# Optimization experiments

Measured on AMD Instinct MI355X. Metric: run time of the kernel, lower is better.

The kernel has to match this reference:

```python
import jax, jax.numpy as jnp
import numpy as np

H = 128   # local_channels (hidden_size)
I = 128   # global_channels (input_size)
T = 30    # future_steps
M = 6     # num_modes
N = 8192  # num agents
MIN_SCALE = 0.001
LN_EPS = 1e-5


def layernorm(x, g, b):
    mu = jnp.mean(x, axis=-1, keepdims=True)
    var = jnp.var(x, axis=-1, keepdims=True)
    return (x - mu) * jax.lax.rsqrt(var + LN_EPS) * g + b


def setup_inputs() -> dict:
    key = jax.random.key(0)
    ks = jax.random.split(key, 24)

    def rn(k, shape, s=0.02):
        return jax.random.normal(k, shape, dtype=jnp.float32) * s

    return {
        "local_embed": jax.random.normal(ks[0], (N, H), jnp.float32),
        "global_embed": jax.random.normal(ks[1], (M, N, I), jnp.float32),
        # GRU params (PyTorch layout: gates ordered r, z, n)
        "W_ih": rn(ks[2], (3 * H, I)), "W_hh": rn(ks[3], (3 * H, H)),
        "b_ih": jnp.zeros((3 * H,), jnp.float32), "b_hh": jnp.zeros((3 * H,), jnp.float32),
        # loc head: Linear(H,H) -> LN -> ReLU -> Linear(H,2)
        "loc1_w": rn(ks[4], (H, H)), "loc1_b": jnp.zeros((H,), jnp.float32),
        "loc_ln_g": jnp.ones((H,), jnp.float32), "loc_ln_b": jnp.zeros((H,), jnp.float32),
        "loc2_w": rn(ks[5], (2, H)), "loc2_b": jnp.zeros((2,), jnp.float32),
        # scale head: same structure
        "sc1_w": rn(ks[6], (H, H)), "sc1_b": jnp.zeros((H,), jnp.float32),
        "sc_ln_g": jnp.ones((H,), jnp.float32), "sc_ln_b": jnp.zeros((H,), jnp.float32),
        "sc2_w": rn(ks[7], (2, H)), "sc2_b": jnp.zeros((2,), jnp.float32),
        # pi head: Linear(H+I,H)->LN->ReLU->Linear(H,H)->LN->ReLU->Linear(H,1)
        "pi1_w": rn(ks[8], (H, H + I)), "pi1_b": jnp.zeros((H,), jnp.float32),
        "pi_ln1_g": jnp.ones((H,), jnp.float32), "pi_ln1_b": jnp.zeros((H,), jnp.float32),
        "pi2_w": rn(ks[9], (H, H)), "pi2_b": jnp.zeros((H,), jnp.float32),
        "pi_ln2_g": jnp.ones((H,), jnp.float32), "pi_ln2_b": jnp.zeros((H,), jnp.float32),
        "pi3_w": rn(ks[10], (1, H)), "pi3_b": jnp.zeros((1,), jnp.float32),
    }


def reference(local_embed, global_embed, W_ih, W_hh, b_ih, b_hh,
              loc1_w, loc1_b, loc_ln_g, loc_ln_b, loc2_w, loc2_b,
              sc1_w, sc1_b, sc_ln_g, sc_ln_b, sc2_w, sc2_b,
              pi1_w, pi1_b, pi_ln1_g, pi_ln1_b, pi2_w, pi2_b,
              pi_ln2_g, pi_ln2_b, pi3_w, pi3_b):
    # pi head: cat(broadcast local [M,N,H], global [M,N,I]) -> MLP -> [N, M]
    pi_in = jnp.concatenate(
        (jnp.broadcast_to(local_embed, (M, N, H)), global_embed), axis=-1)
    h1 = jax.nn.relu(layernorm(pi_in @ pi1_w.T + pi1_b, pi_ln1_g, pi_ln1_b))
    h2 = jax.nn.relu(layernorm(h1 @ pi2_w.T + pi2_b, pi_ln2_g, pi_ln2_b))
    pi = (h2 @ pi3_w.T + pi3_b)[..., 0].T  # [N, M]

    # GRU: input is the SAME x at every timestep -> precompute input gates once
    x = global_embed.reshape(M * N, I)                  # [B, I], B = M*N
    gx = x @ W_ih.T + b_ih                              # [B, 3H]
    xr, xz, xn = jnp.split(gx, 3, axis=-1)
    h0 = jnp.tile(local_embed, (M, 1))                  # [B, H]

    def step(h, _):
        gh = h @ W_hh.T + b_hh
        hr, hz, hn = jnp.split(gh, 3, axis=-1)
        r = jax.nn.sigmoid(xr + hr)
        z = jax.nn.sigmoid(xz + hz)
        n = jnp.tanh(xn + r * hn)
        h_new = (1.0 - z) * n + z * h
        return h_new, h_new

    _, outs = jax.lax.scan(step, h0, None, length=T)    # [T, B, H]
    out = jnp.transpose(outs, (1, 0, 2))                # [B, T, H]

    loc = jax.nn.relu(layernorm(out @ loc1_w.T + loc1_b, loc_ln_g, loc_ln_b)) @ loc2_w.T + loc2_b
    sc = jax.nn.relu(layernorm(out @ sc1_w.T + sc1_b, sc_ln_g, sc_ln_b)) @ sc2_w.T + sc2_b
    scale = jax.nn.elu(sc) + 1.0 + MIN_SCALE

    traj = jnp.concatenate((loc, scale), axis=-1).reshape(M, N, T, 4)
    return traj, pi
```

## Files before the change

kernel.cpp:

```cpp
#include <hip/hip_runtime.h>
#include <math.h>

#define H 128
#define I_DIM 128
#define T_STEPS 30
#define M_MODES 6
#define N_AG 8192
#define B_TOT (M_MODES * N_AG)
#define LN_EPS 1e-5f
#define MIN_SCALE 0.001f
#define LOG2E 1.44269504088896f

typedef short bf16x8 __attribute__((ext_vector_type(8)));
typedef float f32x4 __attribute__((ext_vector_type(4)));

#define MFMA16x16x32(A, B, C) __builtin_amdgcn_mfma_f32_16x16x32_bf16(A, B, C, 0, 0, 0)

__device__ __forceinline__ short f2b(float f) {
    union { float f; unsigned u; } v; v.f = f;
    return (short)((v.u + 0x7FFFu + ((v.u >> 16) & 1u)) >> 16);
}

__device__ __forceinline__ bf16x8 load8_cvt(const float* __restrict__ p) {
    const float4 a = ((const float4*)p)[0];
    const float4 b = ((const float4*)p)[1];
    bf16x8 r;
    r[0]=f2b(a.x); r[1]=f2b(a.y); r[2]=f2b(a.z); r[3]=f2b(a.w);
    r[4]=f2b(b.x); r[5]=f2b(b.y); r[6]=f2b(b.z); r[7]=f2b(b.w);
    return r;
}

__device__ __forceinline__ bf16x8 load8_cvt_s(const float* __restrict__ p, float s) {
    const float4 a = ((const float4*)p)[0];
    const float4 b = ((const float4*)p)[1];
    bf16x8 r;
    r[0]=f2b(a.x*s); r[1]=f2b(a.y*s); r[2]=f2b(a.z*s); r[3]=f2b(a.w*s);
    r[4]=f2b(b.x*s); r[5]=f2b(b.y*s); r[6]=f2b(b.z*s); r[7]=f2b(b.w*s);
    return r;
}

__device__ __forceinline__ float sigm2(float xp) {
    return __builtin_amdgcn_rcpf(1.f + __builtin_amdgcn_exp2f(-xp));
}
__device__ __forceinline__ float tanh2(float yp) {
    return 1.f - 2.f * __builtin_amdgcn_rcpf(1.f + __builtin_amdgcn_exp2f(yp));
}

#define DPP_ADD(v, ctrl)                                                     \
    v += __builtin_bit_cast(float, __builtin_amdgcn_mov_dpp(                 \
             __builtin_bit_cast(int, v), ctrl, 0xF, 0xF, true))

__device__ __forceinline__ float red16(float v) {
    DPP_ADD(v, 0xB1);
    DPP_ADD(v, 0x4E);
    DPP_ADD(v, 0x124);
    DPP_ADD(v, 0x128);
    return v;
}

__global__ __launch_bounds__(256, 2) void gx_kernel(
    const float* __restrict__ global_embed,
    const float* __restrict__ W_ih, const float* __restrict__ b_ih,
    const float* __restrict__ b_hh,
    int base, int ntiles, int Rc, float* __restrict__ gx_ws)
{
    __shared__ short xbuf[16][136];

    const int tid = threadIdx.x;
    const int w  = tid >> 6;
    const int l  = tid & 63;
    const int ln = l & 15;
    const int lg = l >> 4;

    bf16x8 wf[6][4];
    float bias[6];
    #pragma unroll
    for (int nt = 0; nt < 6; ++nt) {
        const int ch = 96*w + 16*nt + ln;
        const float sc = (ch < 2*H) ? LOG2E : (2.f * LOG2E);
        #pragma unroll
        for (int kt = 0; kt < 4; ++kt)
            wf[nt][kt] = load8_cvt_s(W_ih + (size_t)ch * I_DIM + kt*32 + lg*8, sc);
        bias[nt] = (b_ih[ch] + (ch < 2*H ? b_hh[ch] : 0.f)) * sc;
    }

    const int s_r = tid >> 4, s_sg = tid & 15;

    for (int it = blockIdx.x; it < ntiles; it += gridDim.x) {
        const int r0 = it * 16;
        __syncthreads();
        {
            const float* src = global_embed + (size_t)(base + r0 + s_r) * I_DIM + s_sg*8;
            const float4 a = ((const float4*)src)[0];
            const float4 c = ((const float4*)src)[1];
            short tmp[8];
            tmp[0]=f2b(a.x); tmp[1]=f2b(a.y); tmp[2]=f2b(a.z); tmp[3]=f2b(a.w);
            tmp[4]=f2b(c.x); tmp[5]=f2b(c.y); tmp[6]=f2b(c.z); tmp[7]=f2b(c.w);
            *(uint4*)&xbuf[s_r][s_sg*8] = *(uint4*)tmp;
        }
        __syncthreads();

        bf16x8 af[4];
        #pragma unroll
        for (int kt = 0; kt < 4; ++kt)
            af[kt] = *(const bf16x8*)&xbuf[ln][kt*32 + lg*8];

        f32x4 acc[6];
        #pragma unroll
        for (int nt = 0; nt < 6; ++nt) acc[nt] = (f32x4)(0.f);
        #pragma unroll
        for (int kt = 0; kt < 4; ++kt)
            #pragma unroll
            for (int nt = 0; nt < 6; ++nt)
                acc[nt] = MFMA16x16x32(af[kt], wf[nt][kt], acc[nt]);

        #pragma unroll
        for (int nt = 0; nt < 6; ++nt) {
            const f32x4 v = acc[nt] + (f32x4)(bias[nt]);
            *(f32x4*)(gx_ws + (size_t)(96*w + 16*nt + ln) * Rc + r0 + lg*4) = v;
        }
    }
}

#define PI_INBF_OFF   0
#define PI_H1_OFF     33792
#define PI_REDL_OFF   51200
#define PI_RED3_OFF   53248
#define SM_BYTES      54272

__global__ __launch_bounds__(512, 2) void fused_kernel(
    const float* __restrict__ local_embed, const float* __restrict__ gx_ws,
    const float* __restrict__ W_hh, const float* __restrict__ b_hh,
    int base, int ntiles, int Rc, int F,
    const float* __restrict__ loc1_w, const float* __restrict__ loc1_b,
    const float* __restrict__ loc_ln_g, const float* __restrict__ loc_ln_b,
    const float* __restrict__ loc2_w, const float* __restrict__ loc2_b,
    const float* __restrict__ sc1_w, const float* __restrict__ sc1_b,
    const float* __restrict__ sc_ln_g, const float* __restrict__ sc_ln_b,
    const float* __restrict__ sc2_w, const float* __restrict__ sc2_b,
    float* __restrict__ traj,
    const float* __restrict__ global_embed,
    const float* __restrict__ pi1_w, const float* __restrict__ pi1_b,
    const float* __restrict__ ln1_g, const float* __restrict__ ln1_b,
    const float* __restrict__ pi2_w, const float* __restrict__ pi2_b,
    const float* __restrict__ ln2_g, const float* __restrict__ ln2_b,
    const float* __restrict__ pi3_w, const float* __restrict__ pi3_b,
    float* __restrict__ pi_out)
{
    __shared__ __align__(16) char smraw[SM_BYTES];

    const int tid = threadIdx.x;
    const int w  = tid >> 6;
    const int l  = tid & 63;
    const int ln = l & 15;
    const int lg = l >> 4;

    if ((int)blockIdx.x < F) {
        short (*hb0p)[136] = (short(*)[136])smraw;
        short (*hb1p)[136] = (short(*)[136])(smraw + 8704);

        if (w < 4) {
            bf16x8 wf[3][2][4];
            float bhn[2];
            #pragma unroll
            for (int u = 0; u < 2; ++u) {
                const int c = 32*w + 16*u + ln;
                bhn[u] = b_hh[2*H + c] * (2.f * LOG2E);
                #pragma unroll
                for (int g = 0; g < 3; ++g) {
                    const int crow = g*H + c;
                    const float sc = (g < 2) ? LOG2E : (2.f * LOG2E);
                    #pragma unroll
                    for (int kt = 0; kt < 4; ++kt)
                        wf[g][u][kt] = load8_cvt_s(W_hh + (size_t)crow * H + kt*32 + lg*8, sc);
                }
            }

            for (int it = blockIdx.x; it < ntiles; it += F) {
                const int lb0 = it * 32;
                __syncthreads();

                {
                    const int r  = tid >> 3;
                    const int sg = tid & 7;
                    const int b = base + lb0 + r;
                    const int n = b & (N_AG - 1);
                    const float* src = local_embed + (size_t)n * H;
                    #pragma unroll
                    for (int hseg = 0; hseg < 2; ++hseg) {
                        const int s8 = sg + hseg*8;
                        const float4 a = ((const float4*)(src + s8*8))[0];
                        const float4 c = ((const float4*)(src + s8*8))[1];
                        short tmp[8];
                        tmp[0]=f2b(a.x); tmp[1]=f2b(a.y); tmp[2]=f2b(a.z); tmp[3]=f2b(a.w);
                        tmp[4]=f2b(c.x); tmp[5]=f2b(c.y); tmp[6]=f2b(c.z); tmp[7]=f2b(c.w);
                        *(uint4*)&hb0p[r][s8*8] = *(uint4*)tmp;
                    }
                }

                float h_reg[2][2][4];
                #pragma unroll
                for (int grp = 0; grp < 2; ++grp)
                    #pragma unroll
                    for (int u = 0; u < 2; ++u) {
                        const int j = 32*w + 16*u + ln;
                        #pragma unroll
                        for (int rg = 0; rg < 4; ++rg) {
                            const int b = base + lb0 + grp*16 + lg*4 + rg;
                            const int n = b & (N_AG - 1);
                            h_reg[grp][u][rg] = local_embed[(size_t)n * H + j];
                        }
                    }
                float gx[2][3][2][4];
                #pragma unroll
                for (int grp = 0; grp < 2; ++grp)
                    #pragma unroll
                    for (int g = 0; g < 3; ++g)
                        #pragma unroll
                        for (int u = 0; u < 2; ++u) {
                            const int ch = g*128 + 32*w + 16*u + ln;
                            const f32x4 v = *(const f32x4*)(gx_ws + (size_t)ch * Rc + lb0 + grp*16 + lg*4);
                            #pragma unroll
                            for (int rg = 0; rg < 4; ++rg) gx[grp][g][u][rg] = v[rg];
                        }
                __syncthreads();

                int cur = 0;
                for (int i = 0; i <= T_STEPS; ++i) {
                    if (i < T_STEPS) {
                        short (*hc)[136] = cur ? hb1p : hb0p;
                        short (*hx)[136] = cur ? hb0p : hb1p;
                        #pragma unroll
                        for (int grp = 0; grp < 2; ++grp) {
                            bf16x8 af[4];
                            #pragma unroll
                            for (int kt = 0; kt < 4; ++kt)
                                af[kt] = *(const bf16x8*)&hc[grp*16 + ln][kt*32 + lg*8];

                            f32x4 ga[3][2];
                            #pragma unroll
                            for (int g = 0; g < 3; ++g)
                                #pragma unroll
                                for (int u = 0; u < 2; ++u) ga[g][u] = (f32x4)(0.f);
                            #pragma unroll
                            for (int kt = 0; kt < 4; ++kt)
                                #pragma unroll
                                for (int g = 0; g < 3; ++g)
                                    #pragma unroll
                                    for (int u = 0; u < 2; ++u)
                                        ga[g][u] = MFMA16x16x32(af[kt], wf[g][u][kt], ga[g][u]);

                            #pragma unroll
                            for (int u = 0; u < 2; ++u) {
                                const int j = 32*w + 16*u + ln;
                                #pragma unroll
                                for (int rg = 0; rg < 4; ++rg) {
                                    const float rr = sigm2(gx[grp][0][u][rg] + ga[0][u][rg]);
                                    const float zz = sigm2(gx[grp][1][u][rg] + ga[1][u][rg]);
                                    const float nn = tanh2(gx[grp][2][u][rg] + rr * (ga[2][u][rg] + bhn[u]));
                                    const float h  = nn + zz * (h_reg[grp][u][rg] - nn);
                                    h_reg[grp][u][rg] = h;
                                    hx[grp*16 + lg*4 + rg][j] = f2b(h);
                                }
                            }
                        }
                    }
                    __syncthreads();
                    cur ^= 1;
                }
            }
        } else {
            const int hw = w - 4;
            const int hd = hw & 1;
            const int mrow = (hw >> 1) * 16;

            const float* __restrict__ W1  = hd ? sc1_w   : loc1_w;
            const float* __restrict__ B1v = hd ? sc1_b   : loc1_b;
            const float* __restrict__ Gv  = hd ? sc_ln_g : loc_ln_g;
            const float* __restrict__ Bv  = hd ? sc_ln_b : loc_ln_b;
            const float* __restrict__ W2  = hd ? sc2_w   : loc2_w;
            const float* __restrict__ B2v = hd ? sc2_b   : loc2_b;

            bf16x8 whf[8][4];
            float bias1[8], lng[8], lnb[8], w2a[8], w2b[8];
            #pragma unroll
            for (int nt = 0; nt < 8; ++nt) {
                const int c = 16*nt + ln;
                #pragma unroll
                for (int kt = 0; kt < 4; ++kt)
                    whf[nt][kt] = load8_cvt(W1 + (size_t)c * H + kt*32 + lg*8);
                bias1[nt] = B1v[c]; lng[nt] = Gv[c]; lnb[nt] = Bv[c];
                w2a[nt] = W2[c];    w2b[nt] = W2[H + c];
            }
            const float b2_0 = B2v[0], b2_1 = B2v[1];

            for (int it = blockIdx.x; it < ntiles; it += F) {
                const int lb0 = it * 32;
                __syncthreads();
                __syncthreads();

                int cur = 0;
                for (int i = 0; i <= T_STEPS; ++i) {
                    if (i >= 1) {
                        short (*hc)[136] = cur ? hb1p : hb0p;
                        bf16x8 af[4];
                        #pragma unroll
                        for (int kt = 0; kt < 4; ++kt)
                            af[kt] = *(const bf16x8*)&hc[mrow + ln][kt*32 + lg*8];

                        f32x4 acc[8];
                        #pragma unroll
                        for (int nt = 0; nt < 8; ++nt) acc[nt] = (f32x4)(0.f);
                        #pragma unroll
                        for (int kt = 0; kt < 4; ++kt)
                            #pragma unroll
                            for (int nt = 0; nt < 8; ++nt)
                                acc[nt] = MFMA16x16x32(af[kt], whf[nt][kt], acc[nt]);

                        const int t = i - 1;
                        #pragma unroll
                        for (int rg = 0; rg < 4; ++rg) {
                            float s = 0.f, q = 0.f;
                            #pragma unroll
                            for (int nt = 0; nt < 8; ++nt) {
                                const float a = acc[nt][rg] + bias1[nt];
                                acc[nt][rg] = a;
                                s += a; q += a*a;
                            }
                            s = red16(s);
                            q = red16(q);
                            const float mu = s * (1.f/H);
                            const float var = q * (1.f/H) - mu*mu;
                            const float rs = rsqrtf(var + LN_EPS);
                            const float murs = mu * rs;
                            float p0 = 0.f, p1 = 0.f;
                            #pragma unroll
                            for (int nt = 0; nt < 8; ++nt) {
                                float v = fmaf(fmaf(acc[nt][rg], rs, -murs), lng[nt], lnb[nt]);
                                v = fmaxf(v, 0.f);
                                p0 = fmaf(v, w2a[nt], p0);
                                p1 = fmaf(v, w2b[nt], p1);
                            }
                            p0 = red16(p0);
                            p1 = red16(p1);
                            if (ln == 0) {
                                const int b = base + lb0 + mrow + lg*4 + rg;
                                float v0 = p0 + b2_0;
                                float v1 = p1 + b2_1;
                                if (hd) {
                                    v0 = (v0 > 0.f ? v0 : expm1f(v0)) + 1.0f + MIN_SCALE;
                                    v1 = (v1 > 0.f ? v1 : expm1f(v1)) + 1.0f + MIN_SCALE;
                                }
                                *(float2*)(traj + ((size_t)b * T_STEPS + t) * 4 + hd*2) = make_float2(v0, v1);
                            }
                        }
                    }
                    __syncthreads();
                    cur ^= 1;
                }
            }
        }
        return;
    }

    {
        const int pbid = blockIdx.x - F;
        const int pgrid = gridDim.x - F;
        const int sub  = tid >> 8;
        const int stid = tid & 255;
        const int w4 = stid >> 6;

        short (*inbf)[264] = (short(*)[264])(smraw + PI_INBF_OFF + (size_t)sub*16896);
        short (*h1bf)[136] = (short(*)[136])(smraw + PI_H1_OFF   + (size_t)sub*8704);
        float (*redL)[32][2] = (float(*)[32][2])(smraw + PI_REDL_OFF + (size_t)sub*1024);
        float (*red3)[32]    = (float(*)[32])(smraw + PI_RED3_OFF + (size_t)sub*512);

        bf16x8 wf1[2][8];
        bf16x8 wf2[2][4];
        float b1[2], g1[2], bb1[2], b2[2], g2[2], bb2[2], w3[2];
        #pragma unroll
        for (int nt = 0; nt < 2; ++nt) {
            const int c = 32*w4 + 16*nt + ln;
            #pragma unroll
            for (int kt = 0; kt < 8; ++kt)
                wf1[nt][kt] = load8_cvt(pi1_w + (size_t)c * (2*H) + kt*32 + lg*8);
            #pragma unroll
            for (int kt = 0; kt < 4; ++kt)
                wf2[nt][kt] = load8_cvt(pi2_w + (size_t)c * H + kt*32 + lg*8);
            b1[nt] = pi1_b[c]; g1[nt] = ln1_g[c]; bb1[nt] = ln1_b[c];
            b2[nt] = pi2_b[c]; g2[nt] = ln2_g[c]; bb2[nt] = ln2_b[c];
            w3[nt] = pi3_w[c];
        }
        const float b3 = pi3_b[0];

        const int npairs = (B_TOT / 32) / 2;

        for (int p = pbid; p < npairs; p += pgrid) {
            const int r0 = (p*2 + sub) * 32;
            {
                const int r   = stid >> 3;
                const int seg = stid & 7;
                const int b = r0 + r;
                const int n = b & (N_AG - 1);
                const float* src = (seg < 4) ? (local_embed + (size_t)n * H + seg * 32)
                                             : (global_embed + (size_t)b * I_DIM + (seg - 4) * 32);
                short tmp[32];
                #pragma unroll
                for (int i = 0; i < 8; ++i) {
                    const float4 v = ((const float4*)src)[i];
                    tmp[i*4+0]=f2b(v.x); tmp[i*4+1]=f2b(v.y); tmp[i*4+2]=f2b(v.z); tmp[i*4+3]=f2b(v.w);
                }
                #pragma unroll
                for (int i = 0; i < 4; ++i)
                    *(uint4*)&inbf[r][seg*32 + i*8] = *(uint4*)&tmp[i*8];
            }
            __syncthreads();

            f32x4 acc1[2][2];
            #pragma unroll
            for (int m = 0; m < 2; ++m) {
                #pragma unroll
                for (int nt = 0; nt < 2; ++nt) acc1[m][nt] = (f32x4)(0.f);
                bf16x8 af[8];
                #pragma unroll
                for (int kt = 0; kt < 8; ++kt)
                    af[kt] = *(const bf16x8*)&inbf[m*16 + ln][kt*32 + lg*8];
                #pragma unroll
                for (int kt = 0; kt < 8; ++kt)
                    #pragma unroll
                    for (int nt = 0; nt < 2; ++nt)
                        acc1[m][nt] = MFMA16x16x32(af[kt], wf1[nt][kt], acc1[m][nt]);
            }

            #pragma unroll
            for (int m = 0; m < 2; ++m)
                #pragma unroll
                for (int rg = 0; rg < 4; ++rg) {
                    float s = 0.f, q = 0.f;
                    #pragma unroll
                    for (int nt = 0; nt < 2; ++nt) {
                        const float a = acc1[m][nt][rg] + b1[nt];
                        acc1[m][nt][rg] = a;
                        s += a; q += a*a;
                    }
                    s = red16(s);
                    q = red16(q);
                    if (ln == 0) {
                        const int row = m*16 + lg*4 + rg;
                        redL[w4][row][0] = s;
                        redL[w4][row][1] = q;
                    }
                }
            __syncthreads();

            #pragma unroll
            for (int m = 0; m < 2; ++m)
                #pragma unroll
                for (int rg = 0; rg < 4; ++rg) {
                    const int row = m*16 + lg*4 + rg;
                    const float S = redL[0][row][0] + redL[1][row][0] + redL[2][row][0] + redL[3][row][0];
                    const float Q = redL[0][row][1] + redL[1][row][1] + redL[2][row][1] + redL[3][row][1];
                    const float mu = S * (1.f/H);
                    const float var = Q * (1.f/H) - mu*mu;
                    const float rs = rsqrtf(var + LN_EPS);
                    #pragma unroll
                    for (int nt = 0; nt < 2; ++nt) {
                        const float v = fmaxf((acc1[m][nt][rg] - mu) * rs * g1[nt] + bb1[nt], 0.f);
                        h1bf[row][32*w4 + 16*nt + ln] = f2b(v);
                    }
                }
            __syncthreads();

            f32x4 acc2[2][2];
            #pragma unroll
            for (int m = 0; m < 2; ++m) {
                #pragma unroll
                for (int nt = 0; nt < 2; ++nt) acc2[m][nt] = (f32x4)(0.f);
                bf16x8 af[4];
                #pragma unroll
                for (int kt = 0; kt < 4; ++kt)
                    af[kt] = *(const bf16x8*)&h1bf[m*16 + ln][kt*32 + lg*8];
                #pragma unroll
                for (int kt = 0; kt < 4; ++kt)
                    #pragma unroll
                    for (int nt = 0; nt < 2; ++nt)
                        acc2[m][nt] = MFMA16x16x32(af[kt], wf2[nt][kt], acc2[m][nt]);
            }

            #pragma unroll
            for (int m = 0; m < 2; ++m)
                #pragma unroll
                for (int rg = 0; rg < 4; ++rg) {
                    float s = 0.f, q = 0.f;
                    #pragma unroll
                    for (int nt = 0; nt < 2; ++nt) {
                        const float a = acc2[m][nt][rg] + b2[nt];
                        acc2[m][nt][rg] = a;
                        s += a; q += a*a;
                    }
                    s = red16(s);
                    q = red16(q);
                    if (ln == 0) {
                        const int row = m*16 + lg*4 + rg;
                        redL[w4][row][0] = s;
                        redL[w4][row][1] = q;
                    }
                }
            __syncthreads();

            #pragma unroll
            for (int m = 0; m < 2; ++m)
                #pragma unroll
                for (int rg = 0; rg < 4; ++rg) {
                    const int row = m*16 + lg*4 + rg;
                    const float S = redL[0][row][0] + redL[1][row][0] + redL[2][row][0] + redL[3][row][0];
                    const float Q = redL[0][row][1] + redL[1][row][1] + redL[2][row][1] + redL[3][row][1];
                    const float mu = S * (1.f/H);
                    const float var = Q * (1.f/H) - mu*mu;
                    const float rs = rsqrtf(var + LN_EPS);
                    float p2 = 0.f;
                    #pragma unroll
                    for (int nt = 0; nt < 2; ++nt) {
                        const float v = fmaxf((acc2[m][nt][rg] - mu) * rs * g2[nt] + bb2[nt], 0.f);
                        p2 = fmaf(v, w3[nt], p2);
                    }
                    p2 = red16(p2);
                    if (ln == 0) red3[w4][row] = p2;
                }
            __syncthreads();

            if (stid < 32) {
                const int row = stid;
                const float pv = red3[0][row] + red3[1][row] + red3[2][row] + red3[3][row] + b3;
                const int b = r0 + row;
                const int n = b & (N_AG - 1);
                const int m = b >> 13;
                pi_out[(size_t)n * M_MODES + m] = pv;
            }
            __syncthreads();
        }
    }
}

extern "C" void kernel_launch(void* const* d_in, const int* in_sizes, int n_in,
                              void* d_out, int out_size, void* d_ws, size_t ws_size,
                              hipStream_t stream) {
    (void)in_sizes; (void)n_in; (void)out_size;
    const float* local_embed  = (const float*)d_in[0];
    const float* global_embed = (const float*)d_in[1];
    const float* W_ih   = (const float*)d_in[2];
    const float* W_hh   = (const float*)d_in[3];
    const float* b_ih   = (const float*)d_in[4];
    const float* b_hh   = (const float*)d_in[5];
    const float* loc1_w = (const float*)d_in[6];
    const float* loc1_b = (const float*)d_in[7];
    const float* loc_ln_g = (const float*)d_in[8];
    const float* loc_ln_b = (const float*)d_in[9];
    const float* loc2_w = (const float*)d_in[10];
    const float* loc2_b = (const float*)d_in[11];
    const float* sc1_w  = (const float*)d_in[12];
    const float* sc1_b  = (const float*)d_in[13];
    const float* sc_ln_g = (const float*)d_in[14];
    const float* sc_ln_b = (const float*)d_in[15];
    const float* sc2_w  = (const float*)d_in[16];
    const float* sc2_b  = (const float*)d_in[17];
    const float* pi1_w  = (const float*)d_in[18];
    const float* pi1_b  = (const float*)d_in[19];
    const float* pi_ln1_g = (const float*)d_in[20];
    const float* pi_ln1_b = (const float*)d_in[21];
    const float* pi2_w  = (const float*)d_in[22];
    const float* pi2_b  = (const float*)d_in[23];
    const float* pi_ln2_g = (const float*)d_in[24];
    const float* pi_ln2_b = (const float*)d_in[25];
    const float* pi3_w  = (const float*)d_in[26];
    const float* pi3_b  = (const float*)d_in[27];

    float* traj = (float*)d_out;
    float* pi_out = traj + (size_t)B_TOT * T_STEPS * 4;

    const size_t row_bytes = 384 * sizeof(float);
    long long rc = (long long)(ws_size / row_bytes);
    int Rc = rc > B_TOT ? B_TOT : (int)rc;
    Rc &= ~31;

    if (Rc >= 32) {
        float* gx_ws = (float*)d_ws;
        bool first = true;

        for (int basep = 0; basep < B_TOT; basep += Rc) {
            const int rows = (B_TOT - basep < Rc) ? (B_TOT - basep) : Rc;

            const int gxtiles = rows / 16;
            gx_kernel<<<(gxtiles < 512 ? gxtiles : 512), 256, 0, stream>>>(
                global_embed, W_ih, b_ih, b_hh, basep, gxtiles, Rc, gx_ws);

            const int ntiles = rows / 32;
            int F = ntiles < 768 ? ntiles : 768;
            const int P = first ? 256 : 0;
            fused_kernel<<<F + P, 512, 0, stream>>>(
                local_embed, gx_ws, W_hh, b_hh, basep, ntiles, Rc, F,
                loc1_w, loc1_b, loc_ln_g, loc_ln_b, loc2_w, loc2_b,
                sc1_w, sc1_b, sc_ln_g, sc_ln_b, sc2_w, sc2_b, traj,
                global_embed,
                pi1_w, pi1_b, pi_ln1_g, pi_ln1_b,
                pi2_w, pi2_b, pi_ln2_g, pi_ln2_b, pi3_w, pi3_b, pi_out);
            first = false;
        }
    }
}
```

Baseline: 589.2 us.

## Fuse GRU input-gate GEMM into recurrent kernel and drop gx workspace

Removes the separate gx_kernel and its global workspace. Each recurrent tile now stages global_embed in LDS as bf16 (loaded by the head warps) and computes the input gates with MFMA, using W_ih fragments that are then overwritten by W_hh fragments in the same registers. Also switches bf16 conversion to packed v_cvt_pk_bf16_f32 and defers traj stores by one step so they overlap the next timestep. This trades a global round-trip of the 384-wide gx buffer and an extra launch for reloading and converting both weight matrices once per tile.

```diff
diff --git a/kernel.cpp b/kernel.cpp
--- a/kernel.cpp
+++ b/kernel.cpp
@@ -16,27 +16,34 @@
 
 #define MFMA16x16x32(A, B, C) __builtin_amdgcn_mfma_f32_16x16x32_bf16(A, B, C, 0, 0, 0)
 
+__device__ __forceinline__ unsigned cvt_pk(float lo, float hi) {
+    unsigned r;
+    asm("v_cvt_pk_bf16_f32 %0, %1, %2" : "=v"(r) : "v"(lo), "v"(hi));
+    return r;
+}
+
+__device__ __forceinline__ uint4 pack8(float4 a, float4 b) {
+    uint4 r;
+    r.x = cvt_pk(a.x, a.y); r.y = cvt_pk(a.z, a.w);
+    r.z = cvt_pk(b.x, b.y); r.w = cvt_pk(b.z, b.w);
+    return r;
+}
+
+__device__ __forceinline__ bf16x8 load8_cvt(const float* __restrict__ p) {
+    return __builtin_bit_cast(bf16x8, pack8(((const float4*)p)[0], ((const float4*)p)[1]));
+}
+
+__device__ __forceinline__ bf16x8 load8_cvt_s(const float* __restrict__ p, float s) {
+    float4 a = ((const float4*)p)[0];
+    float4 b = ((const float4*)p)[1];
+    a.x*=s; a.y*=s; a.z*=s; a.w*=s;
+    b.x*=s; b.y*=s; b.z*=s; b.w*=s;
+    return __builtin_bit_cast(bf16x8, pack8(a, b));
+}
+
 __device__ __forceinline__ short f2b(float f) {
     union { float f; unsigned u; } v; v.f = f;
     return (short)((v.u + 0x7FFFu + ((v.u >> 16) & 1u)) >> 16);
-}
-
-__device__ __forceinline__ bf16x8 load8_cvt(const float* __restrict__ p) {
-    const float4 a = ((const float4*)p)[0];
-    const float4 b = ((const float4*)p)[1];
-    bf16x8 r;
-    r[0]=f2b(a.x); r[1]=f2b(a.y); r[2]=f2b(a.z); r[3]=f2b(a.w);
-    r[4]=f2b(b.x); r[5]=f2b(b.y); r[6]=f2b(b.z); r[7]=f2b(b.w);
-    return r;
-}
-
-__device__ __forceinline__ bf16x8 load8_cvt_s(const float* __restrict__ p, float s) {
-    const float4 a = ((const float4*)p)[0];
-    const float4 b = ((const float4*)p)[1];
-    bf16x8 r;
-    r[0]=f2b(a.x*s); r[1]=f2b(a.y*s); r[2]=f2b(a.z*s); r[3]=f2b(a.w*s);
-    r[4]=f2b(b.x*s); r[5]=f2b(b.y*s); r[6]=f2b(b.z*s); r[7]=f2b(b.w*s);
-    return r;
 }
 
 __device__ __forceinline__ float sigm2(float xp) {
@@ -58,70 +65,8 @@
     return v;
 }
 
-__global__ __launch_bounds__(256, 2) void gx_kernel(
-    const float* __restrict__ global_embed,
-    const float* __restrict__ W_ih, const float* __restrict__ b_ih,
-    const float* __restrict__ b_hh,
-    int base, int ntiles, int Rc, float* __restrict__ gx_ws)
-{
-    __shared__ short xbuf[16][136];
-
-    const int tid = threadIdx.x;
-    const int w  = tid >> 6;
-    const int l  = tid & 63;
-    const int ln = l & 15;
-    const int lg = l >> 4;
-
-    bf16x8 wf[6][4];
-    float bias[6];
-    #pragma unroll
-    for (int nt = 0; nt < 6; ++nt) {
-        const int ch = 96*w + 16*nt + ln;
-        const float sc = (ch < 2*H) ? LOG2E : (2.f * LOG2E);
-        #pragma unroll
-        for (int kt = 0; kt < 4; ++kt)
-            wf[nt][kt] = load8_cvt_s(W_ih + (size_t)ch * I_DIM + kt*32 + lg*8, sc);
-        bias[nt] = (b_ih[ch] + (ch < 2*H ? b_hh[ch] : 0.f)) * sc;
-    }
-
-    const int s_r = tid >> 4, s_sg = tid & 15;
-
-    for (int it = blockIdx.x; it < ntiles; it += gridDim.x) {
-        const int r0 = it * 16;
-        __syncthreads();
-        {
-            const float* src = global_embed + (size_t)(base + r0 + s_r) * I_DIM + s_sg*8;
-            const float4 a = ((const float4*)src)[0];
-            const float4 c = ((const float4*)src)[1];
-            short tmp[8];
-            tmp[0]=f2b(a.x); tmp[1]=f2b(a.y); tmp[2]=f2b(a.z); tmp[3]=f2b(a.w);
-            tmp[4]=f2b(c.x); tmp[5]=f2b(c.y); tmp[6]=f2b(c.z); tmp[7]=f2b(c.w);
-            *(uint4*)&xbuf[s_r][s_sg*8] = *(uint4*)tmp;
-        }
-        __syncthreads();
-
-        bf16x8 af[4];
-        #pragma unroll
-        for (int kt = 0; kt < 4; ++kt)
-            af[kt] = *(const bf16x8*)&xbuf[ln][kt*32 + lg*8];
-
-        f32x4 acc[6];
-        #pragma unroll
-        for (int nt = 0; nt < 6; ++nt) acc[nt] = (f32x4)(0.f);
-        #pragma unroll
-        for (int kt = 0; kt < 4; ++kt)
-            #pragma unroll
-            for (int nt = 0; nt < 6; ++nt)
-                acc[nt] = MFMA16x16x32(af[kt], wf[nt][kt], acc[nt]);
-
-        #pragma unroll
-        for (int nt = 0; nt < 6; ++nt) {
-            const f32x4 v = acc[nt] + (f32x4)(bias[nt]);
-            *(f32x4*)(gx_ws + (size_t)(96*w + 16*nt + ln) * Rc + r0 + lg*4) = v;
-        }
-    }
-}
-
+#define HB0 0
+#define HB1 8704
 #define PI_INBF_OFF   0
 #define PI_H1_OFF     33792
 #define PI_REDL_OFF   51200
@@ -129,9 +74,10 @@
 #define SM_BYTES      54272
 
 __global__ __launch_bounds__(512, 2) void fused_kernel(
-    const float* __restrict__ local_embed, const float* __restrict__ gx_ws,
-    const float* __restrict__ W_hh, const float* __restrict__ b_hh,
-    int base, int ntiles, int Rc, int F,
+    const float* __restrict__ local_embed, const float* __restrict__ global_embed,
+    const float* __restrict__ W_ih, const float* __restrict__ W_hh,
+    const float* __restrict__ b_ih, const float* __restrict__ b_hh,
+    int ntiles, int F,
     const float* __restrict__ loc1_w, const float* __restrict__ loc1_b,
     const float* __restrict__ loc_ln_g, const float* __restrict__ loc_ln_b,
     const float* __restrict__ loc2_w, const float* __restrict__ loc2_b,
@@ -139,7 +85,6 @@
     const float* __restrict__ sc_ln_g, const float* __restrict__ sc_ln_b,
     const float* __restrict__ sc2_w, const float* __restrict__ sc2_b,
     float* __restrict__ traj,
-    const float* __restrict__ global_embed,
     const float* __restrict__ pi1_w, const float* __restrict__ pi1_b,
     const float* __restrict__ ln1_g, const float* __restrict__ ln1_b,
     const float* __restrict__ pi2_w, const float* __restrict__ pi2_b,
@@ -156,45 +101,38 @@
     const int lg = l >> 4;
 
     if ((int)blockIdx.x < F) {
-        short (*hb0p)[136] = (short(*)[136])smraw;
-        short (*hb1p)[136] = (short(*)[136])(smraw + 8704);
-
         if (w < 4) {
-            bf16x8 wf[3][2][4];
-            float bhn[2];
+            float bias_ih[3][2], bhn[2];
             #pragma unroll
             for (int u = 0; u < 2; ++u) {
                 const int c = 32*w + 16*u + ln;
                 bhn[u] = b_hh[2*H + c] * (2.f * LOG2E);
                 #pragma unroll
                 for (int g = 0; g < 3; ++g) {
-                    const int crow = g*H + c;
                     const float sc = (g < 2) ? LOG2E : (2.f * LOG2E);
-                    #pragma unroll
-                    for (int kt = 0; kt < 4; ++kt)
-                        wf[g][u][kt] = load8_cvt_s(W_hh + (size_t)crow * H + kt*32 + lg*8, sc);
-                }
-            }
+                    bias_ih[g][u] = (b_ih[g*H + c] + (g < 2 ? b_hh[g*H + c] : 0.f)) * sc;
+                }
+            }
+            const int ro = ln*272 + lg*16;
+            const int wb = (lg*4)*272 + (32*w + ln)*2;
+            const int sr_ = tid >> 3;
+            const int ssg = tid & 7;
+
+            bf16x8 wf[3][2][4];
 
             for (int it = blockIdx.x; it < ntiles; it += F) {
                 const int lb0 = it * 32;
                 __syncthreads();
 
                 {
-                    const int r  = tid >> 3;
-                    const int sg = tid & 7;
-                    const int b = base + lb0 + r;
-                    const int n = b & (N_AG - 1);
+                    const int n = (lb0 + sr_) & (N_AG - 1);
                     const float* src = local_embed + (size_t)n * H;
                     #pragma unroll
                     for (int hseg = 0; hseg < 2; ++hseg) {
-                        const int s8 = sg + hseg*8;
+                        const int s8 = ssg + hseg*8;
                         const float4 a = ((const float4*)(src + s8*8))[0];
                         const float4 c = ((const float4*)(src + s8*8))[1];
-                        short tmp[8];
-                        tmp[0]=f2b(a.x); tmp[1]=f2b(a.y); tmp[2]=f2b(a.z); tmp[3]=f2b(a.w);
-                        tmp[4]=f2b(c.x); tmp[5]=f2b(c.y); tmp[6]=f2b(c.z); tmp[7]=f2b(c.w);
-                        *(uint4*)&hb0p[r][s8*8] = *(uint4*)tmp;
+                        *(uint4*)(smraw + HB0 + sr_*272 + s8*16) = pack8(a, c);
                     }
                 }
 
@@ -206,36 +144,72 @@
                         const int j = 32*w + 16*u + ln;
                         #pragma unroll
                         for (int rg = 0; rg < 4; ++rg) {
-                            const int b = base + lb0 + grp*16 + lg*4 + rg;
-                            const int n = b & (N_AG - 1);
+                            const int n = (lb0 + grp*16 + lg*4 + rg) & (N_AG - 1);
                             h_reg[grp][u][rg] = local_embed[(size_t)n * H + j];
                         }
                     }
+
+                #pragma unroll
+                for (int u = 0; u < 2; ++u)
+                    #pragma unroll
+                    for (int g = 0; g < 3; ++g) {
+                        const int crow = g*H + 32*w + 16*u + ln;
+                        const float sc = (g < 2) ? LOG2E : (2.f * LOG2E);
+                        #pragma unroll
+                        for (int kt = 0; kt < 4; ++kt)
+                            wf[g][u][kt] = load8_cvt_s(W_ih + (size_t)crow * I_DIM + kt*32 + lg*8, sc);
+                    }
+                __syncthreads();
+
                 float gx[2][3][2][4];
                 #pragma unroll
-                for (int grp = 0; grp < 2; ++grp)
+                for (int grp = 0; grp < 2; ++grp) {
+                    bf16x8 ax[4];
+                    #pragma unroll
+                    for (int kt = 0; kt < 4; ++kt)
+                        ax[kt] = *(const bf16x8*)(smraw + HB1 + ro + grp*4352 + kt*64);
+                    f32x4 ag[3][2];
                     #pragma unroll
                     for (int g = 0; g < 3; ++g)
                         #pragma unroll
-                        for (int u = 0; u < 2; ++u) {
-                            const int ch = g*128 + 32*w + 16*u + ln;
-                            const f32x4 v = *(const f32x4*)(gx_ws + (size_t)ch * Rc + lb0 + grp*16 + lg*4);
-                            #pragma unroll
-                            for (int rg = 0; rg < 4; ++rg) gx[grp][g][u][rg] = v[rg];
-                        }
+                        for (int u = 0; u < 2; ++u) ag[g][u] = (f32x4)(0.f);
+                    #pragma unroll
+                    for (int kt = 0; kt < 4; ++kt)
+                        #pragma unroll
+                        for (int g = 0; g < 3; ++g)
+                            #pragma unroll
+                            for (int u = 0; u < 2; ++u)
+                                ag[g][u] = MFMA16x16x32(ax[kt], wf[g][u][kt], ag[g][u]);
+                    #pragma unroll
+                    for (int g = 0; g < 3; ++g)
+                        #pragma unroll
+                        for (int u = 0; u < 2; ++u)
+                            #pragma unroll
+                            for (int rg = 0; rg < 4; ++rg)
+                                gx[grp][g][u][rg] = ag[g][u][rg] + bias_ih[g][u];
+                }
+
+                #pragma unroll
+                for (int u = 0; u < 2; ++u)
+                    #pragma unroll
+                    for (int g = 0; g < 3; ++g) {
+                        const int crow = g*H + 32*w + 16*u + ln;
+                        const float sc = (g < 2) ? LOG2E : (2.f * LOG2E);
+                        #pragma unroll
+                        for (int kt = 0; kt < 4; ++kt)
+                            wf[g][u][kt] = load8_cvt_s(W_hh + (size_t)crow * H + kt*32 + lg*8, sc);
+                    }
                 __syncthreads();
 
-                int cur = 0;
+                int rd_off = HB0, wr_off = HB1;
                 for (int i = 0; i <= T_STEPS; ++i) {
                     if (i < T_STEPS) {
-                        short (*hc)[136] = cur ? hb1p : hb0p;
-                        short (*hx)[136] = cur ? hb0p : hb1p;
                         #pragma unroll
                         for (int grp = 0; grp < 2; ++grp) {
                             bf16x8 af[4];
                             #pragma unroll
                             for (int kt = 0; kt < 4; ++kt)
-                                af[kt] = *(const bf16x8*)&hc[grp*16 + ln][kt*32 + lg*8];
+                                af[kt] = *(const bf16x8*)(smraw + rd_off + ro + grp*4352 + kt*64);
 
                             f32x4 ga[3][2];
                             #pragma unroll
@@ -252,7 +226,7 @@
 
                             #pragma unroll
                             for (int u = 0; u < 2; ++u) {
-                                const int j = 32*w + 16*u + ln;
+                                float hv[4];
                                 #pragma unroll
                                 for (int rg = 0; rg < 4; ++rg) {
                                     const float rr = sigm2(gx[grp][0][u][rg] + ga[0][u][rg]);
@@ -260,13 +234,20 @@
                                     const float nn = tanh2(gx[grp][2][u][rg] + rr * (ga[2][u][rg] + bhn[u]));
                                     const float h  = nn + zz * (h_reg[grp][u][rg] - nn);
                                     h_reg[grp][u][rg] = h;
-                                    hx[grp*16 + lg*4 + rg][j] = f2b(h);
+                                    hv[rg] = h;
                                 }
+                                const unsigned p0 = cvt_pk(hv[0], hv[1]);
+                                const unsigned p1 = cvt_pk(hv[2], hv[3]);
+                                const int wa = wr_off + wb + grp*4352 + u*32;
+                                *(short*)(smraw + wa)        = (short)p0;
+                                *(short*)(smraw + wa + 272)  = (short)(p0 >> 16);
+                                *(short*)(smraw + wa + 544)  = (short)p1;
+                                *(short*)(smraw + wa + 816)  = (short)(p1 >> 16);
                             }
                         }
                     }
                     __syncthreads();
-                    cur ^= 1;
+                    rd_off ^= 8704; wr_off ^= 8704;
                 }
             }
         } else {
@@ -293,20 +274,42 @@
                 w2a[nt] = W2[c];    w2b[nt] = W2[H + c];
             }
             const float b2_0 = B2v[0], b2_1 = B2v[1];
+            const int ho = (mrow + ln)*272 + lg*16;
+            const int sr_ = (tid - 256) >> 3;
+            const int ssg = tid & 7;
 
             for (int it = blockIdx.x; it < ntiles; it += F) {
                 const int lb0 = it * 32;
                 __syncthreads();
+
+                {
+                    const float* src = global_embed + (size_t)(lb0 + sr_) * I_DIM;
+                    #pragma unroll
+                    for (int hseg = 0; hseg < 2; ++hseg) {
+                        const int s8 = ssg + hseg*8;
+                        const float4 a = ((const float4*)(src + s8*8))[0];
+                        const float4 c = ((const float4*)(src + s8*8))[1];
+                        *(uint4*)(smraw + HB1 + sr_*272 + s8*16) = pack8(a, c);
+                    }
+                }
                 __syncthreads();
-
-                int cur = 0;
+                __syncthreads();
+
+                int rd_off = HB0;
+                float2 pend[4];
                 for (int i = 0; i <= T_STEPS; ++i) {
+                    if (i >= 2 && ln == 0) {
+                        #pragma unroll
+                        for (int rg = 0; rg < 4; ++rg) {
+                            const int b = lb0 + mrow + lg*4 + rg;
+                            *(float2*)(traj + ((size_t)b * T_STEPS + (i - 2)) * 4 + hd*2) = pend[rg];
+                        }
+                    }
                     if (i >= 1) {
-                        short (*hc)[136] = cur ? hb1p : hb0p;
                         bf16x8 af[4];
                         #pragma unroll
                         for (int kt = 0; kt < 4; ++kt)
-                            af[kt] = *(const bf16x8*)&hc[mrow + ln][kt*32 + lg*8];
+                            af[kt] = *(const bf16x8*)(smraw + rd_off + ho + kt*64);
 
                         f32x4 acc[8];
                         #pragma unroll
@@ -317,7 +320,6 @@
                             for (int nt = 0; nt < 8; ++nt)
                                 acc[nt] = MFMA16x16x32(af[kt], whf[nt][kt], acc[nt]);
 
-                        const int t = i - 1;
                         #pragma unroll
                         for (int rg = 0; rg < 4; ++rg) {
                             float s = 0.f, q = 0.f;
@@ -343,20 +345,24 @@
                             }
                             p0 = red16(p0);
                             p1 = red16(p1);
-                            if (ln == 0) {
-                                const int b = base + lb0 + mrow + lg*4 + rg;
-                                float v0 = p0 + b2_0;
-                                float v1 = p1 + b2_1;
-                                if (hd) {
-                                    v0 = (v0 > 0.f ? v0 : expm1f(v0)) + 1.0f + MIN_SCALE;
-                                    v1 = (v1 > 0.f ? v1 : expm1f(v1)) + 1.0f + MIN_SCALE;
-                                }
-                                *(float2*)(traj + ((size_t)b * T_STEPS + t) * 4 + hd*2) = make_float2(v0, v1);
+                            float v0 = p0 + b2_0;
+                            float v1 = p1 + b2_1;
+                            if (hd) {
+                                v0 = (v0 > 0.f ? v0 : expm1f(v0)) + 1.0f + MIN_SCALE;
+                                v1 = (v1 > 0.f ? v1 : expm1f(v1)) + 1.0f + MIN_SCALE;
                             }
+                            pend[rg] = make_float2(v0, v1);
                         }
                     }
                     __syncthreads();
-                    cur ^= 1;
+                    rd_off ^= 8704;
+                }
+                if (ln == 0) {
+                    #pragma unroll
+                    for (int rg = 0; rg < 4; ++rg) {
+                        const int b = lb0 + mrow + lg*4 + rg;
+                        *(float2*)(traj + ((size_t)b * T_STEPS + (T_STEPS - 1)) * 4 + hd*2) = pend[rg];
+                    }
                 }
             }
         }
@@ -404,15 +410,12 @@
                 const int n = b & (N_AG - 1);
                 const float* src = (seg < 4) ? (local_embed + (size_t)n * H + seg * 32)
                                              : (global_embed + (size_t)b * I_DIM + (seg - 4) * 32);
-                short tmp[32];
-                #pragma unroll
-                for (int i = 0; i < 8; ++i) {
-                    const float4 v = ((const float4*)src)[i];
-                    tmp[i*4+0]=f2b(v.x); tmp[i*4+1]=f2b(v.y); tmp[i*4+2]=f2b(v.z); tmp[i*4+3]=f2b(v.w);
-                }
-                #pragma unroll
-                for (int i = 0; i < 4; ++i)
-                    *(uint4*)&inbf[r][seg*32 + i*8] = *(uint4*)&tmp[i*8];
+                #pragma unroll
+                for (int i = 0; i < 4; ++i) {
+                    const float4 a = ((const float4*)src)[2*i];
+                    const float4 c = ((const float4*)src)[2*i+1];
+                    *(uint4*)&inbf[r][seg*32 + i*8] = pack8(a, c);
+                }
             }
             __syncthreads();
 
@@ -545,7 +548,7 @@
 extern "C" void kernel_launch(void* const* d_in, const int* in_sizes, int n_in,
                               void* d_out, int out_size, void* d_ws, size_t ws_size,
                               hipStream_t stream) {
-    (void)in_sizes; (void)n_in; (void)out_size;
+    (void)in_sizes; (void)n_in; (void)out_size; (void)d_ws; (void)ws_size;
     const float* local_embed  = (const float*)d_in[0];
     const float* global_embed = (const float*)d_in[1];
     const float* W_ih   = (const float*)d_in[2];
@@ -578,33 +581,15 @@
     float* traj = (float*)d_out;
     float* pi_out = traj + (size_t)B_TOT * T_STEPS * 4;
 
-    const size_t row_bytes = 384 * sizeof(float);
-    long long rc = (long long)(ws_size / row_bytes);
-    int Rc = rc > B_TOT ? B_TOT : (int)rc;
-    Rc &= ~31;
-
-    if (Rc >= 32) {
-        float* gx_ws = (float*)d_ws;
-        bool first = true;
-
-        for (int basep = 0; basep < B_TOT; basep += Rc) {
-            const int rows = (B_TOT - basep < Rc) ? (B_TOT - basep) : Rc;
-
-            const int gxtiles = rows / 16;
-            gx_kernel<<<(gxtiles < 512 ? gxtiles : 512), 256, 0, stream>>>(
-                global_embed, W_ih, b_ih, b_hh, basep, gxtiles, Rc, gx_ws);
-
-            const int ntiles = rows / 32;
-            int F = ntiles < 768 ? ntiles : 768;
-            const int P = first ? 256 : 0;
-            fused_kernel<<<F + P, 512, 0, stream>>>(
-                local_embed, gx_ws, W_hh, b_hh, basep, ntiles, Rc, F,
-                loc1_w, loc1_b, loc_ln_g, loc_ln_b, loc2_w, loc2_b,
-                sc1_w, sc1_b, sc_ln_g, sc_ln_b, sc2_w, sc2_b, traj,
-                global_embed,
-                pi1_w, pi1_b, pi_ln1_g, pi_ln1_b,
-                pi2_w, pi2_b, pi_ln2_g, pi_ln2_b, pi3_w, pi3_b, pi_out);
-            first = false;
-        }
-    }
-}
+    const int ntiles = B_TOT / 32;
+    const int F = 768;
+    const int P = 256;
+
+    fused_kernel<<<F + P, 512, 0, stream>>>(
+        local_embed, global_embed, W_ih, W_hh, b_ih, b_hh,
+        ntiles, F,
+        loc1_w, loc1_b, loc_ln_g, loc_ln_b, loc2_w, loc2_b,
+        sc1_w, sc1_b, sc_ln_g, sc_ln_b, sc2_w, sc2_b, traj,
+        pi1_w, pi1_b, pi_ln1_g, pi_ln1_b,
+        pi2_w, pi2_b, pi_ln2_g, pi_ln2_b, pi3_w, pi3_b, pi_out);
+}
```

Measured after the change: 568.2 us. 3.6% less time.
